# Kernel optimization log

Hardware: AMD Instinct MI355X
Metric: run time of the kernel (lower is better)

Reference implementation:

```python
import jax, jax.numpy as jnp
import numpy as np
import math

B, N, C_IN = 4, 512, 32
K = 3            # Chebyshev order -> K+1 polynomial terms
H = 4            # attention heads
OUT_PER_HEAD = 64
ACT_OUT = OUT_PER_HEAD * H  # concat_heads=True


def _prelu(x, a):
    return jnp.where(x >= 0, x, a * x)


def setup_inputs() -> dict:
    key = jax.random.key(0)
    ks = jax.random.split(key, 10)
    stdv = 1.0 / math.sqrt(ACT_OUT)
    inp = {
        "X_real": jax.random.normal(ks[0], (B, N, C_IN), jnp.float32),
        "X_imag": jax.random.normal(ks[1], (B, N, C_IN), jnp.float32),
        "L_real": jax.random.normal(ks[2], (B, K + 1, N, N), jnp.float32),
        "L_imag": jax.random.normal(ks[3], (B, K + 1, N, N), jnp.float32),
        # Chebyshev complex weights, uniform(-stdv, stdv) as in torch init
        "weight_real": jax.random.uniform(ks[4], (K + 1, C_IN, ACT_OUT), jnp.float32, -stdv, stdv),
        "weight_imag": jax.random.uniform(ks[5], (K + 1, C_IN, ACT_OUT), jnp.float32, -stdv, stdv),
        # CVLinear(2*C_IN -> H) complex weight/bias
        "attn_w_real": jax.random.normal(ks[6], (2 * C_IN, H), jnp.float32) * 0.1,
        "attn_w_imag": jax.random.normal(ks[7], (2 * C_IN, H), jnp.float32) * 0.1,
        "attn_b_real": jnp.zeros((H,), jnp.float32),
        "attn_b_imag": jnp.zeros((H,), jnp.float32),
        # CPReLU slopes (PReLU applied to real/imag parts independently)
        "prelu_a_real": jnp.float32(0.25),
        "prelu_a_imag": jnp.float32(0.25),
        "bias_real": jnp.zeros((1, ACT_OUT), jnp.float32),
        "bias_imag": jnp.zeros((1, ACT_OUT), jnp.float32),
    }
    return inp


def reference(X_real, X_imag, L_real, L_imag, weight_real, weight_imag,
              attn_w_real, attn_w_imag, attn_b_real, attn_b_imag,
              prelu_a_real, prelu_a_imag, bias_real, bias_imag):
    C = X_real.shape[-1]
    K1 = weight_real.shape[0]
    # --- attention scores: complex linear on concat([X_i, X_j]) ---
    # split the 2C weight into the X_i half and the X_j half (same math,
    # avoids materializing the B*N*N*2C pairwise concat tensor)
    W1r, W2r = attn_w_real[:C], attn_w_real[C:]
    W1i, W2i = attn_w_imag[:C], attn_w_imag[C:]
    si_re = X_real @ W1r - X_imag @ W1i   # (B,N,H)
    si_im = X_real @ W1i + X_imag @ W1r
    sj_re = X_real @ W2r - X_imag @ W2i
    sj_im = X_real @ W2i + X_imag @ W2r
    # scores[b,i,j,h]
    sc_re = si_re[:, :, None, :] + sj_re[:, None, :, :] + attn_b_real
    sc_im = si_im[:, :, None, :] + sj_im[:, None, :, :] + attn_b_imag
    # CPReLU: PReLU on real/imag independently
    sc_re = _prelu(sc_re, prelu_a_real)
    sc_im = _prelu(sc_im, prelu_a_imag)
    # adjacency mask from |L_real| summed over the K+1 polynomial terms
    mask = (jnp.abs(L_real).sum(axis=1) > 1e-9)[..., None]  # (B,N,N,1)
    NEG = jnp.float32(-1e9)
    re_m = jnp.where(mask, sc_re, NEG)
    im_m = jnp.where(mask, sc_im, NEG)
    attn = jax.nn.softmax(re_m * re_m + im_m * im_m, axis=2)  # softmax over j, (B,N,N,H)
    # --- complex Chebyshev propagation: (L*attn) @ X, per k, per head ---
    lre_xr = jnp.einsum('bknj,bnjh,bjc->bknch', L_real, attn, X_real)
    lim_xi = jnp.einsum('bknj,bnjh,bjc->bknch', L_imag, attn, X_imag)
    lre_xi = jnp.einsum('bknj,bnjh,bjc->bknch', L_real, attn, X_imag)
    lim_xr = jnp.einsum('bknj,bnjh,bjc->bknch', L_imag, attn, X_real)
    LXr = lre_xr - lim_xi
    LXi = lre_xi + lim_xr
    # per-head complex weights: (K+1, C, P, H), out index = p*H + h
    Wr = weight_real.reshape(K1, C, OUT_PER_HEAD, H)
    Wi = weight_imag.reshape(K1, C, OUT_PER_HEAD, H)
    Yre = jnp.einsum('bknch,kcph->bnph', LXr, Wr) - jnp.einsum('bknch,kcph->bnph', LXi, Wi)
    Yim = jnp.einsum('bknch,kcph->bnph', LXr, Wi) + jnp.einsum('bknch,kcph->bnph', LXi, Wr)
    Bsz, Nn = X_real.shape[:2]
    out_re = Yre.reshape(Bsz, Nn, -1) + bias_real
    out_im = Yim.reshape(Bsz, Nn, -1) + bias_imag
    return (out_re, out_im)
```

## Files before the change

kernel.cpp:

```cpp
#include <hip/hip_runtime.h>
#include <hip/hip_bf16.h>

#define BB 4
#define NN 512
#define CC 32
#define KK 4
#define HH 4
#define AOUT 256

#define WS_SI_F   0
#define WS_SII_F  (BB*NN*HH)
#define WS_SJR_F  (2*BB*NN*HH)
#define WS_SJI_F  (3*BB*NN*HH)
#define XT_BASE   131072
#define LX_BASE   393216
#define BRE_BASE  4587520
#define BIM_BASE  4718592

typedef __attribute__((ext_vector_type(8))) short bf16x8;
typedef __attribute__((ext_vector_type(4))) float f32x4;

__device__ __forceinline__ ushort f2bfu(float f){
    union { __hip_bfloat16 h; ushort u; } cv;
    cv.h = __float2bfloat16(f);
    return cv.u;
}
__device__ __forceinline__ short f2bfs(float f){ return (short)f2bfu(f); }
__device__ __forceinline__ float bfu2f(unsigned int u){ return __uint_as_float(u << 16); }

__global__ __launch_bounds__(256) void prep_kernel(
    const float* __restrict__ Xr, const float* __restrict__ Xi,
    const float* __restrict__ AWr, const float* __restrict__ AWi,
    const float* __restrict__ Wr, const float* __restrict__ Wi,
    float* __restrict__ ws, char* __restrict__ wsB)
{
    const int blk = blockIdx.x;
    const int t = threadIdx.x;

    if (blk < 8) {
        int idx = blk*256 + t;
        const float* xr = Xr + (size_t)idx * CC;
        const float* xi = Xi + (size_t)idx * CC;
        float sir[HH] = {0,0,0,0}, sii[HH] = {0,0,0,0};
        float sjr[HH] = {0,0,0,0}, sji[HH] = {0,0,0,0};
        for (int c = 0; c < CC; ++c) {
            float xrc = xr[c], xic = xi[c];
            const float* w1r = AWr + c*HH;
            const float* w1i = AWi + c*HH;
            const float* w2r = AWr + (CC + c)*HH;
            const float* w2i = AWi + (CC + c)*HH;
            #pragma unroll
            for (int h = 0; h < HH; ++h) {
                sir[h] = fmaf(xrc, w1r[h], fmaf(-xic, w1i[h], sir[h]));
                sii[h] = fmaf(xrc, w1i[h], fmaf( xic, w1r[h], sii[h]));
                sjr[h] = fmaf(xrc, w2r[h], fmaf(-xic, w2i[h], sjr[h]));
                sji[h] = fmaf(xrc, w2i[h], fmaf( xic, w2r[h], sji[h]));
            }
        }
        #pragma unroll
        for (int h = 0; h < HH; ++h) {
            ws[WS_SI_F  + idx*HH + h] = sir[h];
            ws[WS_SII_F + idx*HH + h] = sii[h];
            ws[WS_SJR_F + idx*HH + h] = sjr[h];
            ws[WS_SJI_F + idx*HH + h] = sji[h];
        }
    } else if (blk < 40) {
        int bid = (blk - 8)*4 + (t >> 6);
        int part = bid >> 6, b = (bid >> 4) & 3, jb = bid & 15;
        const float* X = part ? Xi : Xr;
        int lane = t & 63;
        int c = lane & 31, jh = lane >> 5;

        unsigned int w[8];
        #pragma unroll
        for (int q = 0; q < 8; ++q) {
            int ji = jh*16 + q*2;
            float f0 = X[((size_t)b*NN + jb*32 + ji  )*CC + c];
            float f1 = X[((size_t)b*NN + jb*32 + ji+1)*CC + c];
            w[q] = (unsigned int)f2bfu(f0) | ((unsigned int)f2bfu(f1) << 16);
        }
        char* tile = wsB + XT_BASE + (((size_t)(part*4 + b)*16 + jb) * 2048);
        uint4* dst = (uint4*)(tile + c*64 + jh*32);
        dst[0] = make_uint4(w[0], w[1], w[2], w[3]);
        dst[1] = make_uint4(w[4], w[5], w[6], w[7]);
    } else {
        int idx = (blk - 40)*256 + t;
        int l  = idx & 63;
        int s  = (idx >> 6) & 7;
        int Nt = (idx >> 9) & 3;
        int h  = idx >> 11;
        int p = Nt*16 + (l & 15), o = p*4 + h;
        int e8 = (l >> 4) * 8;
        unsigned int re_w[4], im_w[4];
        #pragma unroll
        for (int q = 0; q < 4; ++q) {
            unsigned int rw = 0, iw = 0;
            #pragma unroll
            for (int half = 0; half < 2; ++half) {
                int kpos = s*32 + e8 + q*2 + half;
                int ri = kpos >> 7, kk = (kpos >> 5) & 3, c = kpos & 31;
                float wr = Wr[(size_t)(kk*CC + c)*AOUT + o];
                float wi = Wi[(size_t)(kk*CC + c)*AOUT + o];
                unsigned int vre = f2bfu(ri ? -wi : wr);
                unsigned int vim = f2bfu(ri ?  wr : wi);
                rw |= vre << (16*half);
                iw |= vim << (16*half);
            }
            re_w[q] = rw; im_w[q] = iw;
        }
        size_t fo = ((size_t)((h*4 + Nt)*8 + s))*1024 + (size_t)l*16;
        *(uint4*)(wsB + BRE_BASE + fo) = make_uint4(re_w[0], re_w[1], re_w[2], re_w[3]);
        *(uint4*)(wsB + BIM_BASE + fo) = make_uint4(im_w[0], im_w[1], im_w[2], im_w[3]);
    }
}

__global__ __launch_bounds__(128) void cheb_main_kernel(
    const float* __restrict__ Lr_g, const float* __restrict__ Li_g,
    const float* __restrict__ abr, const float* __restrict__ abi,
    const float* __restrict__ par, const float* __restrict__ pai,
    const float* __restrict__ ws, char* __restrict__ wsB)
{
    __shared__ ushort Lf[8][528];
    __shared__ float awf[HH][516];
    __shared__ float wredm[2][HH];
    __shared__ float wreds[2][HH];

    const int bn = blockIdx.x;
    const int b = bn >> 9;
    const int n = bn & (NN - 1);
    const int t = threadIdx.x;
    const int l = t & 63;
    const int w = t >> 6;

    #pragma unroll
    for (int it = 0; it < 8; ++it) {
        int k = it & 3;
        const float* src = (it & 4) ? Li_g : Lr_g;
        size_t goff = (((size_t)b*KK + k)*NN + n)*NN + (size_t)t*4;
        float4 v = *(const float4*)(src + goff);
        ushort4 u;
        u.x = f2bfu(v.x); u.y = f2bfu(v.y); u.z = f2bfu(v.z); u.w = f2bfu(v.w);
        *(ushort4*)&Lf[it][t*4] = u;
    }
    __syncthreads();

    const float a_r = par[0], a_i = pai[0];
    float sir[HH], sii[HH];
    #pragma unroll
    for (int h = 0; h < HH; ++h) {
        sir[h] = ws[WS_SI_F  + bn*HH + h] + abr[h];
        sii[h] = ws[WS_SII_F + bn*HH + h] + abi[h];
    }

    float pmax[HH] = {-INFINITY, -INFINITY, -INFINITY, -INFINITY};
    #pragma unroll
    for (int jj = 0; jj < 4; ++jj) {
        int j = t + jj*128;
        float am = fabsf(bfu2f(Lf[0][j])) + fabsf(bfu2f(Lf[1][j]))
                 + fabsf(bfu2f(Lf[2][j])) + fabsf(bfu2f(Lf[3][j]));
        bool msk = am > 1e-9f;
        const float4 sjr4 = *(const float4*)(ws + WS_SJR_F + ((size_t)b*NN + j)*HH);
        const float4 sji4 = *(const float4*)(ws + WS_SJI_F + ((size_t)b*NN + j)*HH);
        const float* sjrp = (const float*)&sjr4;
        const float* sjip = (const float*)&sji4;
        #pragma unroll
        for (int h = 0; h < HH; ++h) {
            float sr = sir[h] + sjrp[h];
            sr = sr >= 0.f ? sr : a_r * sr;
            float sv = sii[h] + sjip[h];
            sv = sv >= 0.f ? sv : a_i * sv;
            float v;
            if (msk) v = sr*sr + sv*sv;
            else { const float NEG = -1e9f; v = NEG*NEG + NEG*NEG; }
            awf[h][j] = v;
            pmax[h] = fmaxf(pmax[h], v);
        }
    }
    #pragma unroll
    for (int h = 0; h < HH; ++h) {
        #pragma unroll
        for (int off = 32; off > 0; off >>= 1)
            pmax[h] = fmaxf(pmax[h], __shfl_xor(pmax[h], off));
    }
    if (l == 0) { wredm[w][0]=pmax[0]; wredm[w][1]=pmax[1]; wredm[w][2]=pmax[2]; wredm[w][3]=pmax[3]; }
    __syncthreads();
    float hm[HH];
    #pragma unroll
    for (int h = 0; h < HH; ++h) hm[h] = fmaxf(wredm[0][h], wredm[1][h]);

    float psum[HH] = {0,0,0,0};
    #pragma unroll
    for (int jj = 0; jj < 4; ++jj) {
        int j = t + jj*128;
        #pragma unroll
        for (int h = 0; h < HH; ++h) {
            float e = __expf(awf[h][j] - hm[h]);
            awf[h][j] = e;
            psum[h] += e;
        }
    }
    #pragma unroll
    for (int h = 0; h < HH; ++h) {
        #pragma unroll
        for (int off = 32; off > 0; off >>= 1)
            psum[h] += __shfl_xor(psum[h], off);
    }
    if (l == 0) { wreds[w][0]=psum[0]; wreds[w][1]=psum[1]; wreds[w][2]=psum[2]; wreds[w][3]=psum[3]; }
    __syncthreads();
    float inv[HH];
    #pragma unroll
    for (int h = 0; h < HH; ++h) inv[h] = 1.0f / (wreds[0][h] + wreds[1][h]);

    const int r_a = l & 15;
    const int jg  = l >> 4;
    const int k_a = r_a >> 2, h_a = r_a & 3;

    f32x4 acc[8];
    #pragma unroll
    for (int a = 0; a < 8; ++a) acc[a] = (f32x4){0.f,0.f,0.f,0.f};

    const char* xtR = wsB + XT_BASE + ((size_t)(0*4 + b)*16 + w*8)*2048;
    const char* xtI = wsB + XT_BASE + ((size_t)(4   + b)*16 + w*8)*2048;
    const int bofs = (l & 15)*64 + jg*16;

    #pragma unroll 2
    for (int s = 0; s < 8; ++s) {
        const int j0 = w*256 + s*32 + jg*8;
        bf16x8 lr8 = *(const bf16x8*)&Lf[k_a][j0];
        bf16x8 li8 = *(const bf16x8*)&Lf[4 + k_a][j0];
        float aww[8];
        *(float4*)&aww[0] = *(const float4*)&awf[h_a][j0];
        *(float4*)&aww[4] = *(const float4*)&awf[h_a][j0 + 4];

        bf16x8 Ar, Ai;
        #pragma unroll
        for (int e = 0; e < 8; ++e) {
            float lrv = bfu2f((ushort)lr8[e]);
            float liv = bfu2f((ushort)li8[e]);
            Ar[e] = f2bfs(lrv * aww[e]);
            Ai[e] = f2bfs(liv * aww[e]);
        }

        bf16x8 Br0 = *(const bf16x8*)(xtR + s*2048 +        bofs);
        bf16x8 Br1 = *(const bf16x8*)(xtR + s*2048 + 1024 + bofs);
        bf16x8 Bi0 = *(const bf16x8*)(xtI + s*2048 +        bofs);
        bf16x8 Bi1 = *(const bf16x8*)(xtI + s*2048 + 1024 + bofs);

        acc[0] = __builtin_amdgcn_mfma_f32_16x16x32_bf16(Ar, Br0, acc[0], 0, 0, 0);
        acc[1] = __builtin_amdgcn_mfma_f32_16x16x32_bf16(Ar, Br1, acc[1], 0, 0, 0);
        acc[2] = __builtin_amdgcn_mfma_f32_16x16x32_bf16(Ai, Bi0, acc[2], 0, 0, 0);
        acc[3] = __builtin_amdgcn_mfma_f32_16x16x32_bf16(Ai, Bi1, acc[3], 0, 0, 0);
        acc[4] = __builtin_amdgcn_mfma_f32_16x16x32_bf16(Ar, Bi0, acc[4], 0, 0, 0);
        acc[5] = __builtin_amdgcn_mfma_f32_16x16x32_bf16(Ar, Bi1, acc[5], 0, 0, 0);
        acc[6] = __builtin_amdgcn_mfma_f32_16x16x32_bf16(Ai, Br0, acc[6], 0, 0, 0);
        acc[7] = __builtin_amdgcn_mfma_f32_16x16x32_bf16(Ai, Br1, acc[7], 0, 0, 0);
    }
    __syncthreads();

    float* pbuf = &awf[0][0];
    if (w == 1) {
        #pragma unroll
        for (int a = 0; a < 8; ++a)
            #pragma unroll
            for (int r = 0; r < 4; ++r)
                pbuf[(a*4 + r)*64 + l] = acc[a][r];
    }
    __syncthreads();
    if (w == 0) {
        const int kk = l >> 4, lc = l & 15;
        #pragma unroll
        for (int a = 0; a < 8; ++a)
            #pragma unroll
            for (int r = 0; r < 4; ++r)
                acc[a][r] += pbuf[(a*4 + r)*64 + l];
        char* lxp = wsB + LX_BASE + (size_t)bn*2048;
        #pragma unroll
        for (int ct = 0; ct < 2; ++ct) {
            const int c = ct*16 + lc;
            #pragma unroll
            for (int r = 0; r < 4; ++r) {
                float iv = inv[r];
                float vr = (acc[0+ct][r] - acc[2+ct][r]) * iv;
                float vi = (acc[4+ct][r] + acc[6+ct][r]) * iv;
                *(ushort*)(lxp + r*512 +       kk*64 + c*2) = f2bfu(vr);
                *(ushort*)(lxp + r*512 + 256 + kk*64 + c*2) = f2bfu(vi);
            }
        }
    }
}

__global__ __launch_bounds__(256) void out_gemm_kernel(
    const char* __restrict__ wsB,
    const float* __restrict__ bsr, const float* __restrict__ bsi,
    float* __restrict__ out)
{
    const int Mtile = blockIdx.x;
    const int t = threadIdx.x, l = t & 63, h = t >> 6;

    const char* abase = wsB + LX_BASE + ((size_t)(Mtile*16 + (l & 15)))*2048
                        + h*512 + (l >> 4)*16;
    bf16x8 Af[8];
    #pragma unroll
    for (int s = 0; s < 8; ++s) Af[s] = *(const bf16x8*)(abase + s*64);

    #pragma unroll
    for (int Nt = 0; Nt < 4; ++Nt) {
        f32x4 are = (f32x4){0.f,0.f,0.f,0.f};
        f32x4 aim = (f32x4){0.f,0.f,0.f,0.f};
        const size_t fbase = ((size_t)((h*4 + Nt)*8))*1024 + (size_t)l*16;
        const char* bre = wsB + BRE_BASE + fbase;
        const char* bim = wsB + BIM_BASE + fbase;
        #pragma unroll
        for (int s = 0; s < 8; ++s) {
            bf16x8 Br = *(const bf16x8*)(bre + s*1024);
            bf16x8 Bi = *(const bf16x8*)(bim + s*1024);
            are = __builtin_amdgcn_mfma_f32_16x16x32_bf16(Af[s], Br, are, 0, 0, 0);
            aim = __builtin_amdgcn_mfma_f32_16x16x32_bf16(Af[s], Bi, aim, 0, 0, 0);
        }
        const int p = Nt*16 + (l & 15), o = p*4 + h;
        const float vbr = bsr[o], vbi = bsi[o];
        #pragma unroll
        for (int r = 0; r < 4; ++r) {
            int bn = Mtile*16 + (l >> 4)*4 + r;
            out[(size_t)bn*AOUT + o] = are[r] + vbr;
            out[(size_t)BB*NN*AOUT + (size_t)bn*AOUT + o] = aim[r] + vbi;
        }
    }
}

extern "C" void kernel_launch(void* const* d_in, const int* in_sizes, int n_in,
                              void* d_out, int out_size, void* d_ws, size_t ws_size,
                              hipStream_t stream)
{
    const float* Xr  = (const float*)d_in[0];
    const float* Xi  = (const float*)d_in[1];
    const float* Lr  = (const float*)d_in[2];
    const float* Li  = (const float*)d_in[3];
    const float* Wr  = (const float*)d_in[4];
    const float* Wi  = (const float*)d_in[5];
    const float* AWr = (const float*)d_in[6];
    const float* AWi = (const float*)d_in[7];
    const float* abr = (const float*)d_in[8];
    const float* abi = (const float*)d_in[9];
    const float* par = (const float*)d_in[10];
    const float* pai = (const float*)d_in[11];
    const float* bsr = (const float*)d_in[12];
    const float* bsi = (const float*)d_in[13];
    float* ws  = (float*)d_ws;
    char*  wsB = (char*)d_ws;
    float* out = (float*)d_out;

    hipLaunchKernelGGL(prep_kernel, dim3(72), dim3(256), 0, stream,
                       Xr, Xi, AWr, AWi, Wr, Wi, ws, wsB);
    hipLaunchKernelGGL(cheb_main_kernel, dim3(BB*NN), dim3(128), 0, stream,
                       Lr, Li, abr, abi, par, pai, ws, wsB);
    hipLaunchKernelGGL(out_gemm_kernel, dim3(128), dim3(256), 0, stream,
                       wsB, bsr, bsi, out);
}
```

Before: 36.06 us.

## Software-pipeline MFMA loop, compute mask from fp32 L, split output GEMM grid

The main kernel now computes the attention mask from the fp32 L values as they are loaded, and keeps each thread's four scores in registers instead of round-tripping them through shared memory. That removes one barrier and several LDS passes. The MFMA loop is manually double-buffered so step s+1's loads overlap step s's compute. The output GEMM kernel is split into 4x more blocks, one per N-tile, which adds parallelism but reloads the A fragments in each block. The mask now uses unrounded fp32 values rather than bf16-rounded ones, which is a slight semantic change.

```diff
diff --git a/kernel.cpp b/kernel.cpp
--- a/kernel.cpp
+++ b/kernel.cpp
@@ -121,7 +121,7 @@
     const float* __restrict__ ws, char* __restrict__ wsB)
 {
     __shared__ ushort Lf[8][528];
-    __shared__ float awf[HH][516];
+    __shared__ float awf[HH][520];
     __shared__ float wredm[2][HH];
     __shared__ float wreds[2][HH];
 
@@ -131,49 +131,57 @@
     const int t = threadIdx.x;
     const int l = t & 63;
     const int w = t >> 6;
-
+    const int jw = 4*t;
+
+    const float4 si_r4 = *(const float4*)(ws + WS_SI_F  + bn*HH);
+    const float4 si_i4 = *(const float4*)(ws + WS_SII_F + bn*HH);
+    float4 sjr[4], sji[4];
+    #pragma unroll
+    for (int e = 0; e < 4; ++e) {
+        sjr[e] = *(const float4*)(ws + WS_SJR_F + ((size_t)b*NN + jw + e)*HH);
+        sji[e] = *(const float4*)(ws + WS_SJI_F + ((size_t)b*NN + jw + e)*HH);
+    }
+    const float a_r = par[0], a_i = pai[0];
+
+    float am4[4] = {0.f,0.f,0.f,0.f};
     #pragma unroll
     for (int it = 0; it < 8; ++it) {
-        int k = it & 3;
         const float* src = (it & 4) ? Li_g : Lr_g;
-        size_t goff = (((size_t)b*KK + k)*NN + n)*NN + (size_t)t*4;
+        size_t goff = (((size_t)b*KK + (it & 3))*NN + n)*NN + jw;
         float4 v = *(const float4*)(src + goff);
+        if (it < 4) {
+            am4[0] += fabsf(v.x); am4[1] += fabsf(v.y);
+            am4[2] += fabsf(v.z); am4[3] += fabsf(v.w);
+        }
         ushort4 u;
         u.x = f2bfu(v.x); u.y = f2bfu(v.y); u.z = f2bfu(v.z); u.w = f2bfu(v.w);
-        *(ushort4*)&Lf[it][t*4] = u;
-    }
-    __syncthreads();
-
-    const float a_r = par[0], a_i = pai[0];
+        *(ushort4*)&Lf[it][jw] = u;
+    }
+
     float sir[HH], sii[HH];
     #pragma unroll
     for (int h = 0; h < HH; ++h) {
-        sir[h] = ws[WS_SI_F  + bn*HH + h] + abr[h];
-        sii[h] = ws[WS_SII_F + bn*HH + h] + abi[h];
-    }
-
+        sir[h] = ((const float*)&si_r4)[h] + abr[h];
+        sii[h] = ((const float*)&si_i4)[h] + abi[h];
+    }
+    float v[4][HH];
     float pmax[HH] = {-INFINITY, -INFINITY, -INFINITY, -INFINITY};
     #pragma unroll
-    for (int jj = 0; jj < 4; ++jj) {
-        int j = t + jj*128;
-        float am = fabsf(bfu2f(Lf[0][j])) + fabsf(bfu2f(Lf[1][j]))
-                 + fabsf(bfu2f(Lf[2][j])) + fabsf(bfu2f(Lf[3][j]));
-        bool msk = am > 1e-9f;
-        const float4 sjr4 = *(const float4*)(ws + WS_SJR_F + ((size_t)b*NN + j)*HH);
-        const float4 sji4 = *(const float4*)(ws + WS_SJI_F + ((size_t)b*NN + j)*HH);
-        const float* sjrp = (const float*)&sjr4;
-        const float* sjip = (const float*)&sji4;
+    for (int e = 0; e < 4; ++e) {
+        bool msk = am4[e] > 1e-9f;
+        const float* sjrp = (const float*)&sjr[e];
+        const float* sjip = (const float*)&sji[e];
         #pragma unroll
         for (int h = 0; h < HH; ++h) {
             float sr = sir[h] + sjrp[h];
             sr = sr >= 0.f ? sr : a_r * sr;
             float sv = sii[h] + sjip[h];
             sv = sv >= 0.f ? sv : a_i * sv;
-            float v;
-            if (msk) v = sr*sr + sv*sv;
-            else { const float NEG = -1e9f; v = NEG*NEG + NEG*NEG; }
-            awf[h][j] = v;
-            pmax[h] = fmaxf(pmax[h], v);
+            float val;
+            if (msk) val = sr*sr + sv*sv;
+            else { const float NEG = -1e9f; val = NEG*NEG + NEG*NEG; }
+            v[e][h] = val;
+            pmax[h] = fmaxf(pmax[h], val);
         }
     }
     #pragma unroll
@@ -184,20 +192,21 @@
     }
     if (l == 0) { wredm[w][0]=pmax[0]; wredm[w][1]=pmax[1]; wredm[w][2]=pmax[2]; wredm[w][3]=pmax[3]; }
     __syncthreads();
+
     float hm[HH];
     #pragma unroll
     for (int h = 0; h < HH; ++h) hm[h] = fmaxf(wredm[0][h], wredm[1][h]);
 
-    float psum[HH] = {0,0,0,0};
-    #pragma unroll
-    for (int jj = 0; jj < 4; ++jj) {
-        int j = t + jj*128;
-        #pragma unroll
-        for (int h = 0; h < HH; ++h) {
-            float e = __expf(awf[h][j] - hm[h]);
-            awf[h][j] = e;
-            psum[h] += e;
-        }
+    float psum[HH];
+    #pragma unroll
+    for (int h = 0; h < HH; ++h) {
+        float4 ev;
+        ev.x = __expf(v[0][h] - hm[h]);
+        ev.y = __expf(v[1][h] - hm[h]);
+        ev.z = __expf(v[2][h] - hm[h]);
+        ev.w = __expf(v[3][h] - hm[h]);
+        *(float4*)&awf[h][jw] = ev;
+        psum[h] = (ev.x + ev.y) + (ev.z + ev.w);
     }
     #pragma unroll
     for (int h = 0; h < HH; ++h) {
@@ -207,6 +216,7 @@
     }
     if (l == 0) { wreds[w][0]=psum[0]; wreds[w][1]=psum[1]; wreds[w][2]=psum[2]; wreds[w][3]=psum[3]; }
     __syncthreads();
+
     float inv[HH];
     #pragma unroll
     for (int h = 0; h < HH; ++h) inv[h] = 1.0f / (wreds[0][h] + wreds[1][h]);
@@ -223,38 +233,60 @@
     const char* xtI = wsB + XT_BASE + ((size_t)(4   + b)*16 + w*8)*2048;
     const int bofs = (l & 15)*64 + jg*16;
 
-    #pragma unroll 2
-    for (int s = 0; s < 8; ++s) {
-        const int j0 = w*256 + s*32 + jg*8;
-        bf16x8 lr8 = *(const bf16x8*)&Lf[k_a][j0];
-        bf16x8 li8 = *(const bf16x8*)&Lf[4 + k_a][j0];
-        float aww[8];
-        *(float4*)&aww[0] = *(const float4*)&awf[h_a][j0];
-        *(float4*)&aww[4] = *(const float4*)&awf[h_a][j0 + 4];
-
-        bf16x8 Ar, Ai;
-        #pragma unroll
-        for (int e = 0; e < 8; ++e) {
-            float lrv = bfu2f((ushort)lr8[e]);
-            float liv = bfu2f((ushort)li8[e]);
-            Ar[e] = f2bfs(lrv * aww[e]);
-            Ai[e] = f2bfs(liv * aww[e]);
-        }
-
-        bf16x8 Br0 = *(const bf16x8*)(xtR + s*2048 +        bofs);
-        bf16x8 Br1 = *(const bf16x8*)(xtR + s*2048 + 1024 + bofs);
-        bf16x8 Bi0 = *(const bf16x8*)(xtI + s*2048 +        bofs);
-        bf16x8 Bi1 = *(const bf16x8*)(xtI + s*2048 + 1024 + bofs);
-
-        acc[0] = __builtin_amdgcn_mfma_f32_16x16x32_bf16(Ar, Br0, acc[0], 0, 0, 0);
-        acc[1] = __builtin_amdgcn_mfma_f32_16x16x32_bf16(Ar, Br1, acc[1], 0, 0, 0);
-        acc[2] = __builtin_amdgcn_mfma_f32_16x16x32_bf16(Ai, Bi0, acc[2], 0, 0, 0);
-        acc[3] = __builtin_amdgcn_mfma_f32_16x16x32_bf16(Ai, Bi1, acc[3], 0, 0, 0);
-        acc[4] = __builtin_amdgcn_mfma_f32_16x16x32_bf16(Ar, Bi0, acc[4], 0, 0, 0);
-        acc[5] = __builtin_amdgcn_mfma_f32_16x16x32_bf16(Ar, Bi1, acc[5], 0, 0, 0);
-        acc[6] = __builtin_amdgcn_mfma_f32_16x16x32_bf16(Ai, Br0, acc[6], 0, 0, 0);
-        acc[7] = __builtin_amdgcn_mfma_f32_16x16x32_bf16(Ai, Br1, acc[7], 0, 0, 0);
-    }
+#define LOAD_STEP(s, BR0,BR1,BI0,BI1, LR8,LI8, AW0,AW1) do {                  \
+        const int j0_ = w*256 + (s)*32 + jg*8;                                \
+        BR0 = *(const bf16x8*)(xtR + (s)*2048 +        bofs);                 \
+        BR1 = *(const bf16x8*)(xtR + (s)*2048 + 1024 + bofs);                 \
+        BI0 = *(const bf16x8*)(xtI + (s)*2048 +        bofs);                 \
+        BI1 = *(const bf16x8*)(xtI + (s)*2048 + 1024 + bofs);                 \
+        LR8 = *(const bf16x8*)&Lf[k_a][j0_];                                  \
+        LI8 = *(const bf16x8*)&Lf[4 + k_a][j0_];                              \
+        AW0 = *(const float4*)&awf[h_a][j0_];                                 \
+        AW1 = *(const float4*)&awf[h_a][j0_ + 4];                             \
+    } while (0)
+
+#define COMP_STEP(BR0,BR1,BI0,BI1, LR8,LI8, AW0,AW1) do {                     \
+        float aww_[8];                                                        \
+        *(float4*)&aww_[0] = AW0; *(float4*)&aww_[4] = AW1;                   \
+        bf16x8 Ar_, Ai_;                                                      \
+        _Pragma("unroll")                                                     \
+        for (int e_ = 0; e_ < 8; ++e_) {                                      \
+            Ar_[e_] = f2bfs(bfu2f((ushort)LR8[e_]) * aww_[e_]);               \
+            Ai_[e_] = f2bfs(bfu2f((ushort)LI8[e_]) * aww_[e_]);               \
+        }                                                                     \
+        acc[0] = __builtin_amdgcn_mfma_f32_16x16x32_bf16(Ar_, BR0, acc[0],0,0,0); \
+        acc[1] = __builtin_amdgcn_mfma_f32_16x16x32_bf16(Ar_, BR1, acc[1],0,0,0); \
+        acc[2] = __builtin_amdgcn_mfma_f32_16x16x32_bf16(Ai_, BI0, acc[2],0,0,0); \
+        acc[3] = __builtin_amdgcn_mfma_f32_16x16x32_bf16(Ai_, BI1, acc[3],0,0,0); \
+        acc[4] = __builtin_amdgcn_mfma_f32_16x16x32_bf16(Ar_, BI0, acc[4],0,0,0); \
+        acc[5] = __builtin_amdgcn_mfma_f32_16x16x32_bf16(Ar_, BI1, acc[5],0,0,0); \
+        acc[6] = __builtin_amdgcn_mfma_f32_16x16x32_bf16(Ai_, BR0, acc[6],0,0,0); \
+        acc[7] = __builtin_amdgcn_mfma_f32_16x16x32_bf16(Ai_, BR1, acc[7],0,0,0); \
+    } while (0)
+
+    {
+        bf16x8 pBr0,pBr1,pBi0,pBi1,pLr,pLi; float4 pA0,pA1;
+        bf16x8 qBr0,qBr1,qBi0,qBi1,qLr,qLi; float4 qA0,qA1;
+        LOAD_STEP(0, pBr0,pBr1,pBi0,pBi1, pLr,pLi, pA0,pA1);
+        LOAD_STEP(1, qBr0,qBr1,qBi0,qBi1, qLr,qLi, qA0,qA1);
+        COMP_STEP(pBr0,pBr1,pBi0,pBi1, pLr,pLi, pA0,pA1);
+        LOAD_STEP(2, pBr0,pBr1,pBi0,pBi1, pLr,pLi, pA0,pA1);
+        COMP_STEP(qBr0,qBr1,qBi0,qBi1, qLr,qLi, qA0,qA1);
+        LOAD_STEP(3, qBr0,qBr1,qBi0,qBi1, qLr,qLi, qA0,qA1);
+        COMP_STEP(pBr0,pBr1,pBi0,pBi1, pLr,pLi, pA0,pA1);
+        LOAD_STEP(4, pBr0,pBr1,pBi0,pBi1, pLr,pLi, pA0,pA1);
+        COMP_STEP(qBr0,qBr1,qBi0,qBi1, qLr,qLi, qA0,qA1);
+        LOAD_STEP(5, qBr0,qBr1,qBi0,qBi1, qLr,qLi, qA0,qA1);
+        COMP_STEP(pBr0,pBr1,pBi0,pBi1, pLr,pLi, pA0,pA1);
+        LOAD_STEP(6, pBr0,pBr1,pBi0,pBi1, pLr,pLi, pA0,pA1);
+        COMP_STEP(qBr0,qBr1,qBi0,qBi1, qLr,qLi, qA0,qA1);
+        LOAD_STEP(7, qBr0,qBr1,qBi0,qBi1, qLr,qLi, qA0,qA1);
+        COMP_STEP(pBr0,pBr1,pBi0,pBi1, pLr,pLi, pA0,pA1);
+        COMP_STEP(qBr0,qBr1,qBi0,qBi1, qLr,qLi, qA0,qA1);
+    }
+#undef LOAD_STEP
+#undef COMP_STEP
+
     __syncthreads();
 
     float* pbuf = &awf[0][0];
@@ -294,37 +326,32 @@
     const float* __restrict__ bsr, const float* __restrict__ bsi,
     float* __restrict__ out)
 {
-    const int Mtile = blockIdx.x;
+    const int Mtile = blockIdx.x >> 2;
+    const int Nt    = blockIdx.x & 3;
     const int t = threadIdx.x, l = t & 63, h = t >> 6;
 
     const char* abase = wsB + LX_BASE + ((size_t)(Mtile*16 + (l & 15)))*2048
                         + h*512 + (l >> 4)*16;
-    bf16x8 Af[8];
-    #pragma unroll
-    for (int s = 0; s < 8; ++s) Af[s] = *(const bf16x8*)(abase + s*64);
-
-    #pragma unroll
-    for (int Nt = 0; Nt < 4; ++Nt) {
-        f32x4 are = (f32x4){0.f,0.f,0.f,0.f};
-        f32x4 aim = (f32x4){0.f,0.f,0.f,0.f};
-        const size_t fbase = ((size_t)((h*4 + Nt)*8))*1024 + (size_t)l*16;
-        const char* bre = wsB + BRE_BASE + fbase;
-        const char* bim = wsB + BIM_BASE + fbase;
-        #pragma unroll
-        for (int s = 0; s < 8; ++s) {
-            bf16x8 Br = *(const bf16x8*)(bre + s*1024);
-            bf16x8 Bi = *(const bf16x8*)(bim + s*1024);
-            are = __builtin_amdgcn_mfma_f32_16x16x32_bf16(Af[s], Br, are, 0, 0, 0);
-            aim = __builtin_amdgcn_mfma_f32_16x16x32_bf16(Af[s], Bi, aim, 0, 0, 0);
-        }
-        const int p = Nt*16 + (l & 15), o = p*4 + h;
-        const float vbr = bsr[o], vbi = bsi[o];
-        #pragma unroll
-        for (int r = 0; r < 4; ++r) {
-            int bn = Mtile*16 + (l >> 4)*4 + r;
-            out[(size_t)bn*AOUT + o] = are[r] + vbr;
-            out[(size_t)BB*NN*AOUT + (size_t)bn*AOUT + o] = aim[r] + vbi;
-        }
+    f32x4 are = (f32x4){0.f,0.f,0.f,0.f};
+    f32x4 aim = (f32x4){0.f,0.f,0.f,0.f};
+    const size_t fbase = ((size_t)((h*4 + Nt)*8))*1024 + (size_t)l*16;
+    const char* bre = wsB + BRE_BASE + fbase;
+    const char* bim = wsB + BIM_BASE + fbase;
+    #pragma unroll
+    for (int s = 0; s < 8; ++s) {
+        bf16x8 Af = *(const bf16x8*)(abase + s*64);
+        bf16x8 Br = *(const bf16x8*)(bre + s*1024);
+        bf16x8 Bi = *(const bf16x8*)(bim + s*1024);
+        are = __builtin_amdgcn_mfma_f32_16x16x32_bf16(Af, Br, are, 0, 0, 0);
+        aim = __builtin_amdgcn_mfma_f32_16x16x32_bf16(Af, Bi, aim, 0, 0, 0);
+    }
+    const int p = Nt*16 + (l & 15), o = p*4 + h;
+    const float vbr = bsr[o], vbi = bsi[o];
+    #pragma unroll
+    for (int r = 0; r < 4; ++r) {
+        int bn = Mtile*16 + (l >> 4)*4 + r;
+        out[(size_t)bn*AOUT + o] = are[r] + vbr;
+        out[(size_t)BB*NN*AOUT + (size_t)bn*AOUT + o] = aim[r] + vbi;
     }
 }
 
@@ -354,6 +381,6 @@
                        Xr, Xi, AWr, AWi, Wr, Wi, ws, wsB);
     hipLaunchKernelGGL(cheb_main_kernel, dim3(BB*NN), dim3(128), 0, stream,
                        Lr, Li, abr, abi, par, pai, ws, wsB);
-    hipLaunchKernelGGL(out_gemm_kernel, dim3(128), dim3(256), 0, stream,
+    hipLaunchKernelGGL(out_gemm_kernel, dim3(512), dim3(256), 0, stream,
                        wsB, bsr, bsi, out);
 }
```

Measured after the change: 32.06 us, median of 2. 11.1% less time.
